# Kernel tuning notes

Hardware: AMD Instinct MI355X
Metric: run time of the kernel (lower is better)

## Reference

```python
import jax, jax.numpy as jnp
import numpy as np

N_EMB = 1024
N_HEAD = 16
EPS = 1e-5


def _linear_params(key, fan_in, fan_out):
    k1, k2 = jax.random.split(key)
    lim = 1.0 / np.sqrt(fan_in)
    W = jax.random.uniform(k1, (fan_in, fan_out), minval=-lim, maxval=lim, dtype=jnp.float32)
    b = jax.random.uniform(k2, (fan_out,), minval=-lim, maxval=lim, dtype=jnp.float32)
    return W, b


def setup_inputs() -> dict:
    key = jax.random.key(0)
    ks = jax.random.split(key, 8)
    x = jax.random.normal(ks[0], (4, 2048, N_EMB), dtype=jnp.float32)
    Wk, bk = _linear_params(ks[1], N_EMB, N_EMB)
    Wq, bq = _linear_params(ks[2], N_EMB, N_EMB)
    Wv, bv = _linear_params(ks[3], N_EMB, N_EMB)
    Wp, bp = _linear_params(ks[4], N_EMB, N_EMB)
    W1, b1 = _linear_params(ks[5], N_EMB, 4 * N_EMB)
    W2, b2 = _linear_params(ks[6], 4 * N_EMB, N_EMB)
    return {
        "x": x,
        "ln1_g": jnp.ones((N_EMB,), jnp.float32), "ln1_b": jnp.zeros((N_EMB,), jnp.float32),
        "Wk": Wk, "bk": bk, "Wq": Wq, "bq": bq, "Wv": Wv, "bv": bv, "Wp": Wp, "bp": bp,
        "ln2_g": jnp.ones((N_EMB,), jnp.float32), "ln2_b": jnp.zeros((N_EMB,), jnp.float32),
        "W1": W1, "b1": b1, "W2": W2, "b2": b2,
        "cond_len": 256,
    }


def _layernorm(x, g, b):
    mu = jnp.mean(x, axis=-1, keepdims=True)
    var = jnp.mean(jnp.square(x - mu), axis=-1, keepdims=True)
    return (x - mu) * jax.lax.rsqrt(var + EPS) * g + b


def _hybrid_mask(T, cond_len):
    # rows attend to all conditioning columns; causal within the remaining block
    i = jnp.arange(T)[:, None]
    j = jnp.arange(T)[None, :]
    return (j < cond_len) | ((i >= cond_len) & (j >= cond_len) & (j <= i))  # [T,T] bool


def _block(x, ln1_g, ln1_b, Wk, bk, Wq, bq, Wv, bv, Wp, bp, ln2_g, ln2_b, W1, b1, W2, b2, cond_len):
    B, T, C = x.shape
    hd = C // N_HEAD
    h = _layernorm(x, ln1_g, ln1_b)
    # QKV: [B,T,C] -> [B,H,T,hd]
    q = (h @ Wq + bq).reshape(B, T, N_HEAD, hd).transpose(0, 2, 1, 3)
    k = (h @ Wk + bk).reshape(B, T, N_HEAD, hd).transpose(0, 2, 1, 3)
    v = (h @ Wv + bv).reshape(B, T, N_HEAD, hd).transpose(0, 2, 1, 3)
    att = jnp.einsum('bhqd,bhkd->bhqk', q, k) * (1.0 / np.sqrt(hd))
    mask = _hybrid_mask(T, cond_len)
    att = jnp.where(mask, att, -jnp.inf)
    att = jax.nn.softmax(att, axis=-1)
    y = jnp.einsum('bhqk,bhkd->bhqd', att, v)
    y = y.transpose(0, 2, 1, 3).reshape(B, T, C)
    x = x + (y @ Wp + bp)
    h2 = _layernorm(x, ln2_g, ln2_b)
    m = jax.nn.gelu(h2 @ W1 + b1, approximate=False) @ W2 + b2
    return x + m


def reference(x, ln1_g, ln1_b, Wk, bk, Wq, bq, Wv, bv, Wp, bp, ln2_g, ln2_b, W1, b1, W2, b2, cond_len):
    return _block(x, ln1_g, ln1_b, Wk, bk, Wq, bq, Wv, bv, Wp, bp, ln2_g, ln2_b, W1, b1, W2, b2, cond_len)
```

## Files before the change

kernel.cpp:

```cpp
#include <hip/hip_runtime.h>

typedef __bf16 bf16;
typedef __attribute__((ext_vector_type(4))) __bf16 bf16x4;
typedef __attribute__((ext_vector_type(8))) __bf16 bf16x8;
typedef __attribute__((ext_vector_type(4))) float f32x4;

__device__ __forceinline__ void stage16(const bf16* g, bf16* l) {
  __builtin_amdgcn_global_load_lds(
      (const __attribute__((address_space(1))) void*)g,
      (__attribute__((address_space(3))) void*)l, 16, 0, 0);
}

__global__ __launch_bounds__(256)
void transpose_f32_bf16(const float* __restrict__ src, bf16* __restrict__ dst, int R, int C)
{
  __shared__ bf16 tile[32][33];
  const int tx = threadIdx.x & 31, ty = threadIdx.x >> 5;
  const int c0 = blockIdx.x * 32, r0 = blockIdx.y * 32;
#pragma unroll
  for (int i = 0; i < 4; ++i)
    tile[ty + i * 8][tx] = (bf16)src[(size_t)(r0 + ty + i * 8) * C + c0 + tx];
  __syncthreads();
#pragma unroll
  for (int i = 0; i < 4; ++i)
    dst[(size_t)(c0 + ty + i * 8) * R + r0 + tx] = tile[tx][ty + i * 8];
}

__global__ __launch_bounds__(256)
void ln_f32_bf16(const float* __restrict__ x, const float* __restrict__ g,
                 const float* __restrict__ bta, bf16* __restrict__ out)
{
  const int row = blockIdx.x * 4 + (threadIdx.x >> 6);
  const int l = threadIdx.x & 63;
  const float* xr = x + (size_t)row * 1024 + l * 16;
  f32x4 a[4];
#pragma unroll
  for (int i = 0; i < 4; ++i) a[i] = ((const f32x4*)xr)[i];
  float s = 0.f, s2 = 0.f;
#pragma unroll
  for (int i = 0; i < 4; ++i)
#pragma unroll
    for (int jj = 0; jj < 4; ++jj) { float vv = a[i][jj]; s += vv; s2 += vv * vv; }
#pragma unroll
  for (int m = 1; m < 64; m <<= 1) { s += __shfl_xor(s, m); s2 += __shfl_xor(s2, m); }
  const float mu = s * (1.0f / 1024.0f);
  const float var = s2 * (1.0f / 1024.0f) - mu * mu;
  const float rs = rsqrtf(var + 1e-5f);
  f32x4 gv[4], bv[4];
#pragma unroll
  for (int i = 0; i < 4; ++i) {
    gv[i] = ((const f32x4*)(g + l * 16))[i];
    bv[i] = ((const f32x4*)(bta + l * 16))[i];
  }
  bf16x8 o0, o1;
#pragma unroll
  for (int i = 0; i < 8; ++i) {
    float v0 = a[i >> 2][i & 3];
    float v1 = a[2 + (i >> 2)][i & 3];
    o0[i] = (bf16)((v0 - mu) * rs * gv[i >> 2][i & 3] + bv[i >> 2][i & 3]);
    o1[i] = (bf16)((v1 - mu) * rs * gv[2 + (i >> 2)][i & 3] + bv[2 + (i >> 2)][i & 3]);
  }
  bf16* orow = out + (size_t)row * 1024 + l * 16;
  ((bf16x8*)orow)[0] = o0;
  ((bf16x8*)orow)[1] = o1;
}

template <int EPI>
__global__ __launch_bounds__(256)
void gemm_bt(const bf16* __restrict__ A, const bf16* __restrict__ Bt,
             const float* __restrict__ bias, const float* __restrict__ biasK,
             const float* __restrict__ biasV,
             void* __restrict__ out, void* __restrict__ outK, void* __restrict__ outV,
             const float* __restrict__ res, int M, int N, int K)
{
  __shared__ bf16 As[3][128 * 32];
  __shared__ bf16 Bs[3][128 * 32];
  const int tid = threadIdx.x;
  const int l = tid & 63;
  const int w = tid >> 6;
  const int wm = w >> 1, wn = w & 1;
  const int m0 = blockIdx.x * 128;
  const int n0 = blockIdx.y * 128;

  const int srow = tid >> 2;
  const int sG8 = ((tid & 3) ^ ((tid >> 3) & 3)) * 8;
  const bf16* gA = A + (size_t)(m0 + srow) * K + sG8;
  const bf16* gB = Bt + (size_t)(n0 + srow) * K + sG8;
  const int ldsOff = srow * 32 + (tid & 3) * 8;

  const int lrow = l & 15;
  const int rdsl = ((l >> 4) ^ ((lrow >> 1) & 3)) * 8;

  f32x4 acc[4][4] = {};
  const int KT = K >> 5;

#define STAGE(buf, k0)                                            \
  do {                                                            \
    stage16(gA + (k0), &As[buf][ldsOff]);                         \
    stage16(gA + (size_t)64 * K + (k0), &As[buf][2048 + ldsOff]); \
    stage16(gB + (k0), &Bs[buf][ldsOff]);                         \
    stage16(gB + (size_t)64 * K + (k0), &Bs[buf][2048 + ldsOff]); \
  } while (0)

  STAGE(0, 0);
  if (KT > 1) STAGE(1, 32);

  int cur = 0;
  for (int kt = 0; kt < KT; ++kt) {
    const int stg = (cur == 0) ? 2 : cur - 1;
    __builtin_amdgcn_s_barrier();
    if (kt + 2 < KT) {
      STAGE(stg, (kt + 2) << 5);
      asm volatile("s_waitcnt vmcnt(8)" ::: "memory");
    } else if (kt + 1 < KT) {
      asm volatile("s_waitcnt vmcnt(4)" ::: "memory");
    } else {
      asm volatile("s_waitcnt vmcnt(0)" ::: "memory");
    }
    __builtin_amdgcn_sched_barrier(0);
    __builtin_amdgcn_s_barrier();

    bf16x8 af[4], bfv[4];
#pragma unroll
    for (int i = 0; i < 4; ++i)
      af[i] = *(const bf16x8*)&As[cur][(wm * 64 + i * 16 + lrow) * 32 + rdsl];
#pragma unroll
    for (int i = 0; i < 4; ++i)
      bfv[i] = *(const bf16x8*)&Bs[cur][(wn * 64 + i * 16 + lrow) * 32 + rdsl];
#pragma unroll
    for (int mi = 0; mi < 4; ++mi)
#pragma unroll
      for (int ni = 0; ni < 4; ++ni)
        acc[mi][ni] = __builtin_amdgcn_mfma_f32_16x16x32_bf16(af[mi], bfv[ni], acc[mi][ni], 0, 0, 0);
    cur = (cur == 2) ? 0 : cur + 1;
  }
#undef STAGE

  const int seg = n0 >> 10;
  const float* bp = (EPI == 0) ? (seg == 0 ? bias : (seg == 1 ? biasK : biasV)) : bias;
#pragma unroll
  for (int mi = 0; mi < 4; ++mi) {
#pragma unroll
    for (int ni = 0; ni < 4; ++ni) {
      const int colg = n0 + wn * 64 + ni * 16 + lrow;
      const int col = (EPI == 0) ? (colg & 1023) : colg;
      const float bv = bp[col];
#pragma unroll
      for (int j = 0; j < 4; ++j) {
        const int row = m0 + wm * 64 + mi * 16 + (l >> 4) * 4 + j;
        float val = acc[mi][ni][j] + bv;
        if constexpr (EPI == 0) {
          const int b = row >> 11, t = row & 2047, hh = col >> 6, d = col & 63;
          if (seg == 0)
            ((bf16*)out)[(((size_t)(b * 16 + hh) * 2048 + t) * 64) + d] = (bf16)(val * 0.125f);
          else if (seg == 1)
            ((bf16*)outK)[(((size_t)(b * 16 + hh) * 2048 + t) * 64) + d] = (bf16)val;
          else
            ((bf16*)outV)[(((size_t)(b * 16 + hh) * 64 + d) * 2048) + t] = (bf16)val;
        } else if constexpr (EPI == 3) {
          ((float*)out)[(size_t)row * 1024 + col] = val + res[(size_t)row * 1024 + col];
        } else if constexpr (EPI == 4) {
          const float u = 0.7978845608f * (val + 0.044715f * val * val * val);
          const float e = __expf(2.0f * u);
          const float th = 1.0f - 2.0f / (e + 1.0f);
          const float ge = 0.5f * val * (1.0f + th);
          ((bf16*)out)[(size_t)row * N + col] = (bf16)ge;
        } else if constexpr (EPI == 5) {
          ((float*)out)[(size_t)row * 1024 + col] = val + res[(size_t)row * 1024 + col];
        }
      }
    }
  }
}

__global__ __launch_bounds__(512)
void attn_kernel(const bf16* __restrict__ q, const bf16* __restrict__ k,
                 const bf16* __restrict__ v, bf16* __restrict__ y,
                 const int* __restrict__ condp)
{
  __shared__ bf16 Ks[2][64 * 72];
  __shared__ bf16 Vs[2][64 * 72];
  __shared__ char PsB[8][2048];
  const int tid = threadIdx.x, l = tid & 63, w = tid >> 6;
  const int bx = blockIdx.x;
  const int qt = 15 - (bx >> 6);
  const int bh = bx & 63;
  const int bb = bh >> 4, hh = bh & 15;
  const int cond = condp[0];
  const int iLo = qt * 128;
  const size_t base = (size_t)bh * 2048 * 64;

  const int lrow = l & 15;
  const int g = l >> 4;
  const int lslot = g * 8;

  const int qrow = iLo + w * 16 + lrow;
  const bf16x8 bq0 = *(const bf16x8*)(q + base + (size_t)qrow * 64 + lslot);
  const bf16x8 bq1 = *(const bf16x8*)(q + base + (size_t)qrow * 64 + 32 + lslot);

  f32x4 o[4] = {};
  float m = -1e30f, lsum = 0.f;

  const int ckt = (cond + 63) >> 6;
  int nkt = ((iLo + 127) >> 6) + 1;
  if (nkt < ckt) nkt = ckt;
  const int wHi = iLo + w * 16 + 15;

  const int kr = tid >> 3;
  const int ks8 = (tid & 7) * 8;
  const bf16* kp = k + base + (size_t)kr * 64 + ks8;
  const bf16* vp = v + base + (size_t)kr * 2048 + ks8;

  bf16x8 rk = *(const bf16x8*)kp;
  bf16x8 rv = *(const bf16x8*)vp;
  *(bf16x8*)&Ks[0][kr * 72 + ks8] = rk;
  *(bf16x8*)&Vs[0][kr * 72 + ks8] = rv;
  __syncthreads();

  char* psw = PsB[w];

  for (int kt = 0; kt < nkt; ++kt) {
    const int cur = kt & 1;
    const int j0 = kt << 6;
    const bool pf = (kt + 1 < nkt);
    if (pf) {
      rk = *(const bf16x8*)(kp + (size_t)(j0 + 64) * 64);
      rv = *(const bf16x8*)(vp + j0 + 64);
    }

    const bool active = (j0 < cond) || (j0 <= wHi);
    if (active) {
      f32x4 sfr[4];
      __builtin_amdgcn_s_setprio(1);
#pragma unroll
      for (int nf = 0; nf < 4; ++nf) {
        f32x4 s = {};
        bf16x8 ka0 = *(const bf16x8*)&Ks[cur][(nf * 16 + lrow) * 72 + lslot];
        bf16x8 ka1 = *(const bf16x8*)&Ks[cur][(nf * 16 + lrow) * 72 + 32 + lslot];
        s = __builtin_amdgcn_mfma_f32_16x16x32_bf16(ka0, bq0, s, 0, 0, 0);
        s = __builtin_amdgcn_mfma_f32_16x16x32_bf16(ka1, bq1, s, 0, 0, 0);
        sfr[nf] = s;
      }
      __builtin_amdgcn_s_setprio(0);

      const bool safe = (j0 + 63 < cond) || (j0 + 63 <= iLo + w * 16);
      if (!safe) {
#pragma unroll
        for (int nf = 0; nf < 4; ++nf)
#pragma unroll
          for (int j = 0; j < 4; ++j) {
            const int kc = j0 + nf * 16 + g * 4 + j;
            const bool ok = (kc < cond) || (kc <= qrow);
            sfr[nf][j] = ok ? sfr[nf][j] : -1e30f;
          }
      }

      float pmax = sfr[0][0];
#pragma unroll
      for (int nf = 0; nf < 4; ++nf)
#pragma unroll
        for (int j = 0; j < 4; ++j) pmax = fmaxf(pmax, sfr[nf][j]);
      pmax = fmaxf(pmax, __shfl_xor(pmax, 16));
      pmax = fmaxf(pmax, __shfl_xor(pmax, 32));

      const bool resc = !__all(pmax - m <= 8.0f);
      if (resc) {
        const float mnew = fmaxf(m, pmax);
        const float alpha = __expf(m - mnew);
        m = mnew;
        lsum *= alpha;
        float ar[4];
#pragma unroll
        for (int j = 0; j < 4; ++j) ar[j] = __shfl(alpha, (l & 48) | (g * 4 + j));
#pragma unroll
        for (int df = 0; df < 4; ++df)
#pragma unroll
          for (int j = 0; j < 4; ++j) o[df][j] *= ar[j];
      }

      float rsum = 0.f;
#pragma unroll
      for (int nf = 0; nf < 4; ++nf) {
        bf16x4 pk;
#pragma unroll
        for (int j = 0; j < 4; ++j) {
          const float p = __expf(sfr[nf][j] - m);
          rsum += p;
          pk[j] = (bf16)p;
        }
        const int slot = 2 * nf + (g >> 1);
        const int boff = lrow * 128 + ((slot ^ (lrow & 7)) << 4) + (g & 1) * 8;
        *(bf16x4*)(psw + boff) = pk;
      }
      rsum += __shfl_xor(rsum, 16);
      rsum += __shfl_xor(rsum, 32);
      lsum += rsum;

      const int r0b = lrow * 128 + (((g) ^ (lrow & 7)) << 4);
      const int r1b = lrow * 128 + (((g + 4) ^ (lrow & 7)) << 4);
      const bf16x8 pa0 = *(const bf16x8*)(psw + r0b);
      const bf16x8 pa1 = *(const bf16x8*)(psw + r1b);
      __builtin_amdgcn_s_setprio(1);
#pragma unroll
      for (int df = 0; df < 4; ++df) {
        bf16x8 v0 = *(const bf16x8*)&Vs[cur][(df * 16 + lrow) * 72 + lslot];
        bf16x8 v1 = *(const bf16x8*)&Vs[cur][(df * 16 + lrow) * 72 + 32 + lslot];
        o[df] = __builtin_amdgcn_mfma_f32_16x16x32_bf16(pa0, v0, o[df], 0, 0, 0);
        o[df] = __builtin_amdgcn_mfma_f32_16x16x32_bf16(pa1, v1, o[df], 0, 0, 0);
      }
      __builtin_amdgcn_s_setprio(0);
    }

    if (pf) {
      *(bf16x8*)&Ks[cur ^ 1][kr * 72 + ks8] = rk;
      *(bf16x8*)&Vs[cur ^ 1][kr * 72 + ks8] = rv;
    }
    __syncthreads();
  }

  float lr[4];
#pragma unroll
  for (int j = 0; j < 4; ++j) lr[j] = 1.0f / __shfl(lsum, (l & 48) | (g * 4 + j));
#pragma unroll
  for (int df = 0; df < 4; ++df)
#pragma unroll
    for (int j = 0; j < 4; ++j) {
      const int irow = iLo + w * 16 + g * 4 + j;
      y[((size_t)bb * 2048 + irow) * 1024 + hh * 64 + df * 16 + lrow] = (bf16)(o[df][j] * lr[j]);
    }
}

extern "C" void kernel_launch(void* const* d_in, const int* in_sizes, int n_in,
                              void* d_out, int out_size, void* d_ws, size_t ws_size,
                              hipStream_t stream) {
  const float* x    = (const float*)d_in[0];
  const float* ln1g = (const float*)d_in[1];
  const float* ln1b = (const float*)d_in[2];
  const float* Wk   = (const float*)d_in[3];
  const float* bk   = (const float*)d_in[4];
  const float* Wq   = (const float*)d_in[5];
  const float* bq   = (const float*)d_in[6];
  const float* Wv   = (const float*)d_in[7];
  const float* bv   = (const float*)d_in[8];
  const float* Wp   = (const float*)d_in[9];
  const float* bpb  = (const float*)d_in[10];
  const float* ln2g = (const float*)d_in[11];
  const float* ln2b = (const float*)d_in[12];
  const float* W1   = (const float*)d_in[13];
  const float* b1   = (const float*)d_in[14];
  const float* W2   = (const float*)d_in[15];
  const float* b2   = (const float*)d_in[16];
  const int*  cond  = (const int*)d_in[17];
  float* out = (float*)d_out;

  char* ws = (char*)d_ws;
  const size_t MB = 1024ull * 1024ull;
  if (ws_size < 136 * MB) return;

  bf16*  WqkvT = (bf16*)(ws + 0 * MB);
  bf16*  WpT   = (bf16*)(ws + 6 * MB);
  bf16*  W1T   = (bf16*)(ws + 8 * MB);
  bf16*  W2T   = (bf16*)(ws + 16 * MB);
  float* x2    = (float*)(ws + 24 * MB);
  bf16*  hbuf  = (bf16*)(ws + 56 * MB);
  bf16*  qb    = (bf16*)(ws + 72 * MB);
  bf16*  kb    = (bf16*)(ws + 88 * MB);
  bf16*  vb    = (bf16*)(ws + 104 * MB);
  bf16*  yb    = (bf16*)(ws + 120 * MB);
  bf16*  m1    = (bf16*)(ws + 72 * MB);

  dim3 blk(256);
  transpose_f32_bf16<<<dim3(32, 32), blk, 0, stream>>>(Wq, WqkvT,                1024, 1024);
  transpose_f32_bf16<<<dim3(32, 32), blk, 0, stream>>>(Wk, WqkvT + 1024 * 1024,  1024, 1024);
  transpose_f32_bf16<<<dim3(32, 32), blk, 0, stream>>>(Wv, WqkvT + 2048 * 1024,  1024, 1024);
  transpose_f32_bf16<<<dim3(32, 32), blk, 0, stream>>>(Wp, WpT, 1024, 1024);
  transpose_f32_bf16<<<dim3(128, 32), blk, 0, stream>>>(W1, W1T, 1024, 4096);
  transpose_f32_bf16<<<dim3(32, 128), blk, 0, stream>>>(W2, W2T, 4096, 1024);

  ln_f32_bf16<<<2048, blk, 0, stream>>>(x, ln1g, ln1b, hbuf);

  gemm_bt<0><<<dim3(64, 24), blk, 0, stream>>>(hbuf, WqkvT, bq, bk, bv,
                                               qb, kb, vb, nullptr, 8192, 3072, 1024);

  attn_kernel<<<dim3(1024), dim3(512), 0, stream>>>(qb, kb, vb, yb, cond);

  gemm_bt<3><<<dim3(64, 8), blk, 0, stream>>>(yb, WpT, bpb, nullptr, nullptr,
                                              x2, nullptr, nullptr, x, 8192, 1024, 1024);
  ln_f32_bf16<<<2048, blk, 0, stream>>>(x2, ln2g, ln2b, hbuf);
  gemm_bt<4><<<dim3(64, 32), blk, 0, stream>>>(hbuf, W1T, b1, nullptr, nullptr,
                                               m1, nullptr, nullptr, nullptr, 8192, 4096, 1024);
  gemm_bt<5><<<dim3(64, 8), blk, 0, stream>>>(m1, W2T, b2, nullptr, nullptr,
                                              out, nullptr, nullptr, x2, 8192, 1024, 4096);
}
```

Before: 409.5 us.

## Add 256x256-tile 8-wave GEMM with interleaved LDS staging for QKV, proj, FC1

Introduces a new GEMM kernel using 256x256 output tiles, 512 threads, BK=64 with double-buffered XOR-swizzled LDS. It splits each k-step into four phases that interleave next-tile staging with MFMA bursts, raising MFMA priority with setprio. The QKV, output-projection and FC1 GEMMs switch to it, while FC2 stays on the older 128x128 kernel, now trimmed to its one epilogue. The larger tiles aim to raise arithmetic intensity and hide global loads. In exchange they raise register pressure and leave fewer blocks for the 8192x1024 GEMMs, which could underfill the GPU.

```diff
diff --git a/kernel.cpp b/kernel.cpp
--- a/kernel.cpp
+++ b/kernel.cpp
@@ -66,11 +66,165 @@
 }
 
 template <int EPI>
-__global__ __launch_bounds__(256)
-void gemm_bt(const bf16* __restrict__ A, const bf16* __restrict__ Bt,
+__global__ __launch_bounds__(512, 2)
+void gemm256(const bf16* __restrict__ A, const bf16* __restrict__ Bt,
              const float* __restrict__ bias, const float* __restrict__ biasK,
              const float* __restrict__ biasV,
              void* __restrict__ out, void* __restrict__ outK, void* __restrict__ outV,
+             const float* __restrict__ res, int M, int N, int K)
+{
+  __shared__ bf16 As[2][256][64];
+  __shared__ bf16 Bs[2][256][64];
+  const int tid = threadIdx.x;
+  const int l = tid & 63;
+  const int w = tid >> 6;
+  const int wm = w >> 2;
+  const int wn = w & 3;
+  const int m0 = blockIdx.x * 256;
+  const int n0 = blockIdx.y * 256;
+
+  const int sr = tid >> 3;
+  const int sl = tid & 7;
+  const int sc = ((sl ^ (sr & 7)) << 3);
+  const bf16* gAr = A + (size_t)(m0 + sr) * K + sc;
+  const bf16* gBr = Bt + (size_t)(n0 + sr) * K + sc;
+
+  const int KT = K >> 6;
+  const int lrow = l & 15;
+  const int g4 = l >> 4;
+
+  f32x4 acc[8][4] = {};
+  bf16x8 a[4][2], b[4][2];
+
+  auto stage_half = [&](int tile, int hh) {
+    const int buf = tile & 1;
+    const int kb = tile << 6;
+    if (hh < 2) {
+      const bf16* g = gAr + (size_t)(hh << 7) * K + kb;
+      stage16(g, &As[buf][(hh << 7) + sr][sl << 3]);
+      stage16(g + (size_t)64 * K, &As[buf][(hh << 7) + 64 + sr][sl << 3]);
+    } else {
+      const int h2 = hh - 2;
+      const bf16* g = gBr + (size_t)(h2 << 7) * K + kb;
+      stage16(g, &Bs[buf][(h2 << 7) + sr][sl << 3]);
+      stage16(g + (size_t)64 * K, &Bs[buf][(h2 << 7) + 64 + sr][sl << 3]);
+    }
+  };
+
+#define RA(mi, dst_i, ks)                                                   \
+  { const int r_ = (wm << 7) + ((mi) << 4) + lrow;                          \
+    a[dst_i][ks] = *(const bf16x8*)&As[buf][r_][((((ks) << 2) + g4) ^ (r_ & 7)) << 3]; }
+#define RB(ni, ks)                                                          \
+  { const int r_ = (wn << 6) + ((ni) << 4) + lrow;                          \
+    b[ni][ks] = *(const bf16x8*)&Bs[buf][r_][((((ks) << 2) + g4) ^ (r_ & 7)) << 3]; }
+
+  stage_half(0, 0); stage_half(0, 1); stage_half(0, 2); stage_half(0, 3);
+  asm volatile("s_waitcnt vmcnt(0)" ::: "memory");
+  __builtin_amdgcn_sched_barrier(0);
+  __builtin_amdgcn_s_barrier();
+
+  for (int kt = 0; kt < KT; ++kt) {
+    const int buf = kt & 1;
+    const bool pf = (kt + 1 < KT);
+#pragma unroll
+    for (int mi = 0; mi < 4; ++mi) { RA(mi, mi, 0); RA(mi, mi, 1); }
+    RB(0, 0); RB(0, 1); RB(1, 0); RB(1, 1);
+    if (pf) stage_half(kt + 1, 0);
+    __builtin_amdgcn_s_barrier();
+    __builtin_amdgcn_s_setprio(1);
+#pragma unroll
+    for (int mi = 0; mi < 4; ++mi)
+#pragma unroll
+      for (int ni = 0; ni < 2; ++ni)
+#pragma unroll
+        for (int ks = 0; ks < 2; ++ks)
+          acc[mi][ni] = __builtin_amdgcn_mfma_f32_16x16x32_bf16(a[mi][ks], b[ni][ks], acc[mi][ni], 0, 0, 0);
+    __builtin_amdgcn_s_setprio(0);
+    __builtin_amdgcn_s_barrier();
+    RB(2, 0); RB(2, 1); RB(3, 0); RB(3, 1);
+    if (pf) stage_half(kt + 1, 1);
+    __builtin_amdgcn_s_barrier();
+    __builtin_amdgcn_s_setprio(1);
+#pragma unroll
+    for (int mi = 0; mi < 4; ++mi)
+#pragma unroll
+      for (int ni = 2; ni < 4; ++ni)
+#pragma unroll
+        for (int ks = 0; ks < 2; ++ks)
+          acc[mi][ni] = __builtin_amdgcn_mfma_f32_16x16x32_bf16(a[mi][ks], b[ni][ks], acc[mi][ni], 0, 0, 0);
+    __builtin_amdgcn_s_setprio(0);
+    __builtin_amdgcn_s_barrier();
+#pragma unroll
+    for (int mi = 0; mi < 4; ++mi) { RA(4 + mi, mi, 0); RA(4 + mi, mi, 1); }
+    if (pf) stage_half(kt + 1, 2);
+    __builtin_amdgcn_s_barrier();
+    __builtin_amdgcn_s_setprio(1);
+#pragma unroll
+    for (int mi = 0; mi < 4; ++mi)
+#pragma unroll
+      for (int ni = 0; ni < 2; ++ni)
+#pragma unroll
+        for (int ks = 0; ks < 2; ++ks)
+          acc[4 + mi][ni] = __builtin_amdgcn_mfma_f32_16x16x32_bf16(a[mi][ks], b[ni][ks], acc[4 + mi][ni], 0, 0, 0);
+    __builtin_amdgcn_s_setprio(0);
+    __builtin_amdgcn_s_barrier();
+    if (pf) stage_half(kt + 1, 3);
+    __builtin_amdgcn_s_setprio(1);
+#pragma unroll
+    for (int mi = 0; mi < 4; ++mi)
+#pragma unroll
+      for (int ni = 2; ni < 4; ++ni)
+#pragma unroll
+        for (int ks = 0; ks < 2; ++ks)
+          acc[4 + mi][ni] = __builtin_amdgcn_mfma_f32_16x16x32_bf16(a[mi][ks], b[ni][ks], acc[4 + mi][ni], 0, 0, 0);
+    __builtin_amdgcn_s_setprio(0);
+    if (pf) {
+      asm volatile("s_waitcnt vmcnt(0)" ::: "memory");
+      __builtin_amdgcn_sched_barrier(0);
+    }
+    __builtin_amdgcn_s_barrier();
+  }
+#undef RA
+#undef RB
+
+  const int seg = n0 >> 10;
+  const float* bp = (EPI == 0) ? (seg == 0 ? bias : (seg == 1 ? biasK : biasV)) : bias;
+#pragma unroll
+  for (int mi = 0; mi < 8; ++mi) {
+#pragma unroll
+    for (int ni = 0; ni < 4; ++ni) {
+      const int colg = n0 + wn * 64 + ni * 16 + lrow;
+      const int col = (EPI == 0) ? (colg & 1023) : colg;
+      const float bv = bp[col];
+#pragma unroll
+      for (int j = 0; j < 4; ++j) {
+        const int row = m0 + wm * 128 + mi * 16 + (l >> 4) * 4 + j;
+        float val = acc[mi][ni][j] + bv;
+        if constexpr (EPI == 0) {
+          const int bb = row >> 11, t = row & 2047, hh = col >> 6, d = col & 63;
+          if (seg == 0)
+            ((bf16*)out)[(((size_t)(bb * 16 + hh) * 2048 + t) * 64) + d] = (bf16)(val * 0.125f);
+          else if (seg == 1)
+            ((bf16*)outK)[(((size_t)(bb * 16 + hh) * 2048 + t) * 64) + d] = (bf16)val;
+          else
+            ((bf16*)outV)[(((size_t)(bb * 16 + hh) * 64 + d) * 2048) + t] = (bf16)val;
+        } else if constexpr (EPI == 3) {
+          ((float*)out)[(size_t)row * 1024 + col] = val + res[(size_t)row * 1024 + col];
+        } else if constexpr (EPI == 4) {
+          const float u = 0.7978845608f * (val + 0.044715f * val * val * val);
+          const float e = __expf(2.0f * u);
+          const float th = 1.0f - 2.0f / (e + 1.0f);
+          ((bf16*)out)[(size_t)row * N + col] = (bf16)(0.5f * val * (1.0f + th));
+        }
+      }
+    }
+  }
+}
+
+template <int EPI>
+__global__ __launch_bounds__(256)
+void gemm_bt(const bf16* __restrict__ A, const bf16* __restrict__ Bt,
+             const float* __restrict__ bias, void* __restrict__ out,
              const float* __restrict__ res, int M, int N, int K)
 {
   __shared__ bf16 As[3][128 * 32];
@@ -136,36 +290,17 @@
   }
 #undef STAGE
 
-  const int seg = n0 >> 10;
-  const float* bp = (EPI == 0) ? (seg == 0 ? bias : (seg == 1 ? biasK : biasV)) : bias;
 #pragma unroll
   for (int mi = 0; mi < 4; ++mi) {
 #pragma unroll
     for (int ni = 0; ni < 4; ++ni) {
-      const int colg = n0 + wn * 64 + ni * 16 + lrow;
-      const int col = (EPI == 0) ? (colg & 1023) : colg;
-      const float bv = bp[col];
+      const int col = n0 + wn * 64 + ni * 16 + lrow;
+      const float bv = bias[col];
 #pragma unroll
       for (int j = 0; j < 4; ++j) {
         const int row = m0 + wm * 64 + mi * 16 + (l >> 4) * 4 + j;
         float val = acc[mi][ni][j] + bv;
-        if constexpr (EPI == 0) {
-          const int b = row >> 11, t = row & 2047, hh = col >> 6, d = col & 63;
-          if (seg == 0)
-            ((bf16*)out)[(((size_t)(b * 16 + hh) * 2048 + t) * 64) + d] = (bf16)(val * 0.125f);
-          else if (seg == 1)
-            ((bf16*)outK)[(((size_t)(b * 16 + hh) * 2048 + t) * 64) + d] = (bf16)val;
-          else
-            ((bf16*)outV)[(((size_t)(b * 16 + hh) * 64 + d) * 2048) + t] = (bf16)val;
-        } else if constexpr (EPI == 3) {
-          ((float*)out)[(size_t)row * 1024 + col] = val + res[(size_t)row * 1024 + col];
-        } else if constexpr (EPI == 4) {
-          const float u = 0.7978845608f * (val + 0.044715f * val * val * val);
-          const float e = __expf(2.0f * u);
-          const float th = 1.0f - 2.0f / (e + 1.0f);
-          const float ge = 0.5f * val * (1.0f + th);
-          ((bf16*)out)[(size_t)row * N + col] = (bf16)ge;
-        } else if constexpr (EPI == 5) {
+        if constexpr (EPI == 5) {
           ((float*)out)[(size_t)row * 1024 + col] = val + res[(size_t)row * 1024 + col];
         }
       }
@@ -379,16 +514,15 @@
 
   ln_f32_bf16<<<2048, blk, 0, stream>>>(x, ln1g, ln1b, hbuf);
 
-  gemm_bt<0><<<dim3(64, 24), blk, 0, stream>>>(hbuf, WqkvT, bq, bk, bv,
-                                               qb, kb, vb, nullptr, 8192, 3072, 1024);
+  gemm256<0><<<dim3(32, 12), dim3(512), 0, stream>>>(hbuf, WqkvT, bq, bk, bv,
+                                                     qb, kb, vb, nullptr, 8192, 3072, 1024);
 
   attn_kernel<<<dim3(1024), dim3(512), 0, stream>>>(qb, kb, vb, yb, cond);
 
-  gemm_bt<3><<<dim3(64, 8), blk, 0, stream>>>(yb, WpT, bpb, nullptr, nullptr,
-                                              x2, nullptr, nullptr, x, 8192, 1024, 1024);
+  gemm256<3><<<dim3(32, 4), dim3(512), 0, stream>>>(yb, WpT, bpb, nullptr, nullptr,
+                                                    x2, nullptr, nullptr, x, 8192, 1024, 1024);
   ln_f32_bf16<<<2048, blk, 0, stream>>>(x2, ln2g, ln2b, hbuf);
-  gemm_bt<4><<<dim3(64, 32), blk, 0, stream>>>(hbuf, W1T, b1, nullptr, nullptr,
-                                               m1, nullptr, nullptr, nullptr, 8192, 4096, 1024);
-  gemm_bt<5><<<dim3(64, 8), blk, 0, stream>>>(m1, W2T, b2, nullptr, nullptr,
-                                              out, nullptr, nullptr, x2, 8192, 1024, 4096);
-}
+  gemm256<4><<<dim3(32, 16), dim3(512), 0, stream>>>(hbuf, W1T, b1, nullptr, nullptr,
+                                                     m1, nullptr, nullptr, nullptr, 8192, 4096, 1024);
+  gemm_bt<5><<<dim3(64, 8), blk, 0, stream>>>(m1, W2T, b2, out, x2, 8192, 1024, 4096);
+}
```

Measured after the change: 422.6 us. 1.03x slower.

## Add 256x256-tile 512-thread GEMM for QKV and FC1 projections

Applied to the files above, without the earlier changes.

Introduces a new GEMM kernel with 256x256 output tiles, 8 waves, and double-buffered LDS staging. It is used for the wide QKV and FC1 GEMMs to raise arithmetic intensity and cut global/LDS traffic per FLOP, and it adds s_setprio around the MFMA block. The older 128-tile kernel is slimmed to the residual epilogues only. Risks are fewer blocks (384/512) relative to the number of CUs, higher register pressure from the 8x4 accumulators, and double instead of triple buffering.

```diff
diff --git a/kernel.cpp b/kernel.cpp
--- a/kernel.cpp
+++ b/kernel.cpp
@@ -66,11 +66,110 @@
 }
 
 template <int EPI>
+__global__ __launch_bounds__(512, 4)
+void gemm256b(const bf16* __restrict__ A, const bf16* __restrict__ Bt,
+              const float* __restrict__ bias, const float* __restrict__ biasK,
+              const float* __restrict__ biasV,
+              void* __restrict__ out, void* __restrict__ outK, void* __restrict__ outV,
+              int M, int N, int K)
+{
+  __shared__ bf16 As[2][256 * 32];
+  __shared__ bf16 Bs[2][256 * 32];
+  const int tid = threadIdx.x;
+  const int l = tid & 63;
+  const int w = tid >> 6;
+  const int wm = w >> 2;
+  const int wn = w & 3;
+  const int m0 = blockIdx.x * 256;
+  const int n0 = blockIdx.y * 256;
+
+  const int srow = tid >> 2;
+  const int sG8 = ((tid & 3) ^ ((tid >> 3) & 3)) * 8;
+  const bf16* gA = A + (size_t)(m0 + srow) * K + sG8;
+  const bf16* gB = Bt + (size_t)(n0 + srow) * K + sG8;
+  const int ldsOff = srow * 32 + (tid & 3) * 8;
+
+  const int lrow = l & 15;
+  const int rdsl = ((l >> 4) ^ ((lrow >> 1) & 3)) * 8;
+
+  f32x4 acc[8][4] = {};
+  const int KT = K >> 5;
+
+#define STAGE(buf, k0)                                                 \
+  do {                                                                 \
+    stage16(gA + (k0), &As[buf][ldsOff]);                              \
+    stage16(gA + (size_t)128 * K + (k0), &As[buf][4096 + ldsOff]);     \
+    stage16(gB + (k0), &Bs[buf][ldsOff]);                              \
+    stage16(gB + (size_t)128 * K + (k0), &Bs[buf][4096 + ldsOff]);     \
+  } while (0)
+
+  STAGE(0, 0);
+
+  for (int kt = 0; kt < KT; ++kt) {
+    const int cur = kt & 1;
+    __builtin_amdgcn_s_barrier();
+    if (kt + 1 < KT) {
+      STAGE(cur ^ 1, (kt + 1) << 5);
+      asm volatile("s_waitcnt vmcnt(4)" ::: "memory");
+    } else {
+      asm volatile("s_waitcnt vmcnt(0)" ::: "memory");
+    }
+    __builtin_amdgcn_sched_barrier(0);
+    __builtin_amdgcn_s_barrier();
+
+    bf16x8 a[8], b[4];
+#pragma unroll
+    for (int mi = 0; mi < 8; ++mi)
+      a[mi] = *(const bf16x8*)&As[cur][(wm * 128 + mi * 16 + lrow) * 32 + rdsl];
+#pragma unroll
+    for (int ni = 0; ni < 4; ++ni)
+      b[ni] = *(const bf16x8*)&Bs[cur][(wn * 64 + ni * 16 + lrow) * 32 + rdsl];
+    __builtin_amdgcn_s_setprio(1);
+#pragma unroll
+    for (int mi = 0; mi < 8; ++mi)
+#pragma unroll
+      for (int ni = 0; ni < 4; ++ni)
+        acc[mi][ni] = __builtin_amdgcn_mfma_f32_16x16x32_bf16(a[mi], b[ni], acc[mi][ni], 0, 0, 0);
+    __builtin_amdgcn_s_setprio(0);
+  }
+#undef STAGE
+
+  const int seg = n0 >> 10;
+  const float* bp = (EPI == 0) ? (seg == 0 ? bias : (seg == 1 ? biasK : biasV)) : bias;
+#pragma unroll
+  for (int mi = 0; mi < 8; ++mi) {
+#pragma unroll
+    for (int ni = 0; ni < 4; ++ni) {
+      const int colg = n0 + wn * 64 + ni * 16 + lrow;
+      const int col = (EPI == 0) ? (colg & 1023) : colg;
+      const float bv = bp[col];
+#pragma unroll
+      for (int j = 0; j < 4; ++j) {
+        const int row = m0 + wm * 128 + mi * 16 + (l >> 4) * 4 + j;
+        float val = acc[mi][ni][j] + bv;
+        if constexpr (EPI == 0) {
+          const int bb = row >> 11, t = row & 2047, hh = col >> 6, d = col & 63;
+          if (seg == 0)
+            ((bf16*)out)[(((size_t)(bb * 16 + hh) * 2048 + t) * 64) + d] = (bf16)(val * 0.125f);
+          else if (seg == 1)
+            ((bf16*)outK)[(((size_t)(bb * 16 + hh) * 2048 + t) * 64) + d] = (bf16)val;
+          else
+            ((bf16*)outV)[(((size_t)(bb * 16 + hh) * 64 + d) * 2048) + t] = (bf16)val;
+        } else if constexpr (EPI == 4) {
+          const float u = 0.7978845608f * (val + 0.044715f * val * val * val);
+          const float e = __expf(2.0f * u);
+          const float th = 1.0f - 2.0f / (e + 1.0f);
+          ((bf16*)out)[(size_t)row * N + col] = (bf16)(0.5f * val * (1.0f + th));
+        }
+      }
+    }
+  }
+}
+
+template <int EPI>
 __global__ __launch_bounds__(256)
 void gemm_bt(const bf16* __restrict__ A, const bf16* __restrict__ Bt,
-             const float* __restrict__ bias, const float* __restrict__ biasK,
-             const float* __restrict__ biasV,
-             void* __restrict__ out, void* __restrict__ outK, void* __restrict__ outV,
+             const float* __restrict__ bias, void* __restrict__ out,
              const float* __restrict__ res, int M, int N, int K)
 {
   __shared__ bf16 As[3][128 * 32];
@@ -136,36 +235,17 @@
   }
 #undef STAGE
 
-  const int seg = n0 >> 10;
-  const float* bp = (EPI == 0) ? (seg == 0 ? bias : (seg == 1 ? biasK : biasV)) : bias;
 #pragma unroll
   for (int mi = 0; mi < 4; ++mi) {
 #pragma unroll
     for (int ni = 0; ni < 4; ++ni) {
-      const int colg = n0 + wn * 64 + ni * 16 + lrow;
-      const int col = (EPI == 0) ? (colg & 1023) : colg;
-      const float bv = bp[col];
+      const int col = n0 + wn * 64 + ni * 16 + lrow;
+      const float bv = bias[col];
 #pragma unroll
       for (int j = 0; j < 4; ++j) {
         const int row = m0 + wm * 64 + mi * 16 + (l >> 4) * 4 + j;
         float val = acc[mi][ni][j] + bv;
-        if constexpr (EPI == 0) {
-          const int b = row >> 11, t = row & 2047, hh = col >> 6, d = col & 63;
-          if (seg == 0)
-            ((bf16*)out)[(((size_t)(b * 16 + hh) * 2048 + t) * 64) + d] = (bf16)(val * 0.125f);
-          else if (seg == 1)
-            ((bf16*)outK)[(((size_t)(b * 16 + hh) * 2048 + t) * 64) + d] = (bf16)val;
-          else
-            ((bf16*)outV)[(((size_t)(b * 16 + hh) * 64 + d) * 2048) + t] = (bf16)val;
-        } else if constexpr (EPI == 3) {
-          ((float*)out)[(size_t)row * 1024 + col] = val + res[(size_t)row * 1024 + col];
-        } else if constexpr (EPI == 4) {
-          const float u = 0.7978845608f * (val + 0.044715f * val * val * val);
-          const float e = __expf(2.0f * u);
-          const float th = 1.0f - 2.0f / (e + 1.0f);
-          const float ge = 0.5f * val * (1.0f + th);
-          ((bf16*)out)[(size_t)row * N + col] = (bf16)ge;
-        } else if constexpr (EPI == 5) {
+        if constexpr (EPI == 3 || EPI == 5) {
           ((float*)out)[(size_t)row * 1024 + col] = val + res[(size_t)row * 1024 + col];
         }
       }
@@ -379,16 +459,14 @@
 
   ln_f32_bf16<<<2048, blk, 0, stream>>>(x, ln1g, ln1b, hbuf);
 
-  gemm_bt<0><<<dim3(64, 24), blk, 0, stream>>>(hbuf, WqkvT, bq, bk, bv,
-                                               qb, kb, vb, nullptr, 8192, 3072, 1024);
+  gemm256b<0><<<dim3(32, 12), dim3(512), 0, stream>>>(hbuf, WqkvT, bq, bk, bv,
+                                                      qb, kb, vb, 8192, 3072, 1024);
 
   attn_kernel<<<dim3(1024), dim3(512), 0, stream>>>(qb, kb, vb, yb, cond);
 
-  gemm_bt<3><<<dim3(64, 8), blk, 0, stream>>>(yb, WpT, bpb, nullptr, nullptr,
-                                              x2, nullptr, nullptr, x, 8192, 1024, 1024);
+  gemm_bt<3><<<dim3(64, 8), blk, 0, stream>>>(yb, WpT, bpb, x2, x, 8192, 1024, 1024);
   ln_f32_bf16<<<2048, blk, 0, stream>>>(x2, ln2g, ln2b, hbuf);
-  gemm_bt<4><<<dim3(64, 32), blk, 0, stream>>>(hbuf, W1T, b1, nullptr, nullptr,
-                                               m1, nullptr, nullptr, nullptr, 8192, 4096, 1024);
-  gemm_bt<5><<<dim3(64, 8), blk, 0, stream>>>(m1, W2T, b2, nullptr, nullptr,
-                                              out, nullptr, nullptr, x2, 8192, 1024, 4096);
-}
+  gemm256b<4><<<dim3(32, 16), dim3(512), 0, stream>>>(hbuf, W1T, b1, nullptr, nullptr,
+                                                      m1, nullptr, nullptr, 8192, 4096, 1024);
+  gemm_bt<5><<<dim3(64, 8), blk, 0, stream>>>(m1, W2T, b2, out, x2, 8192, 1024, 4096);
+}
```

Result: slower. 1.491 ms (+264.1%).
